# Optimization experiments

Hardware: AMD Instinct MI355X
Metric: run time of the kernel (lower is better)

The kernel has to match this reference:

```python
import jax, jax.numpy as jnp
import numpy as np

NEG_SLOPE = 0.01  # nn.LeakyReLU default


def _quantize_weight(w, bits):
    """Brevitas-style per-tensor symmetric narrow-range weight quantization.
    scale = max|w| / (2^(bits-1)-1); w_q = clip(round(w/scale)) * scale."""
    n = float(2 ** (bits - 1) - 1)
    scale = jnp.max(jnp.abs(w)) / n
    q = jnp.clip(jnp.round(w / scale), -n, n)
    return q * scale


def setup_inputs() -> dict:
    key = jax.random.key(0)
    ks = jax.random.split(key, 7)
    N, D_in, D_out = 32768, 1024, 2048
    x = jax.random.normal(ks[0], (N, D_in), dtype=jnp.float32)
    # He-ish init scaling for stability
    W0 = jax.random.normal(ks[1], (D_out, D_in), dtype=jnp.float32) * (1.0 / np.sqrt(D_in))
    b0 = jax.random.normal(ks[2], (D_out,), dtype=jnp.float32) * 0.01
    W1 = jax.random.normal(ks[3], (D_out, D_out), dtype=jnp.float32) * (1.0 / np.sqrt(D_out))
    b1 = jax.random.normal(ks[4], (D_out,), dtype=jnp.float32) * 0.01
    W2 = jax.random.normal(ks[5], (D_out, D_out), dtype=jnp.float32) * (1.0 / np.sqrt(D_out))
    b2 = jax.random.normal(ks[6], (D_out,), dtype=jnp.float32) * 0.01
    return {"x": x, "W0": W0, "b0": b0, "W1": W1, "b1": b1, "W2": W2, "b2": b2}


def reference(x, W0, b0, W1, b1, W2, b2):
    # Layer 0: QuantLinear with default 8-bit weights, then LeakyReLU, dropout(p=0)=id
    h = jnp.dot(x, _quantize_weight(W0, 8).T) + b0
    h = jnp.where(h >= 0, h, NEG_SLOPE * h)
    # Layers 1..2: 4-bit quantized weights
    for W, b in ((W1, b1), (W2, b2)):
        h = jnp.dot(h, _quantize_weight(W, 4).T) + b
        h = jnp.where(h >= 0, h, NEG_SLOPE * h)
    return h
```

## Files before the change

### kernel.cpp

```cpp
#include <hip/hip_runtime.h>
#include <hip/hip_bf16.h>
#include <stdint.h>

typedef __bf16 bf16x8 __attribute__((ext_vector_type(8)));
typedef float  f32x4  __attribute__((ext_vector_type(4)));
typedef unsigned short u16;

__device__ __forceinline__ u16 f2bf(float f) {
    return __builtin_bit_cast(u16, __float2bfloat16(f));
}

__device__ __forceinline__ void gload16(const void* g, void* l) {
    __builtin_amdgcn_global_load_lds(
        (const __attribute__((address_space(1))) void*)g,
        (__attribute__((address_space(3))) void*)l,
        16, 0, 0);
}


__global__ void zero3_k(unsigned int* p) {
    if (threadIdx.x < 3) p[threadIdx.x] = 0u;
}

__global__ void maxabs_k(const float* __restrict__ w, int n, unsigned int* __restrict__ out) {
    const int tid = threadIdx.x;
    float m = 0.f;
    for (int i = blockIdx.x * blockDim.x + tid; i < n; i += gridDim.x * blockDim.x)
        m = fmaxf(m, fabsf(w[i]));
    #pragma unroll
    for (int off = 32; off > 0; off >>= 1)
        m = fmaxf(m, __shfl_down(m, off));
    __shared__ float red[4];
    if ((tid & 63) == 0) red[tid >> 6] = m;
    __syncthreads();
    if (tid == 0) {
        m = fmaxf(fmaxf(red[0], red[1]), fmaxf(red[2], red[3]));
        atomicMax(out, __float_as_uint(m));
    }
}

__global__ void quant_k(const float* __restrict__ w, int n,
                        const unsigned int* __restrict__ maxbits, float qn,
                        u16* __restrict__ out) {
    const float scale = __uint_as_float(*maxbits) / qn;
    for (int i = blockIdx.x * blockDim.x + threadIdx.x; i < n; i += gridDim.x * blockDim.x) {
        float q = rintf(w[i] / scale);
        q = fminf(qn, fmaxf(-qn, q));
        out[i] = f2bf(q * scale);
    }
}

__global__ void cvt_k(const float* __restrict__ x, u16* __restrict__ o, long n) {
    const long stride = (long)gridDim.x * blockDim.x * 4;
    for (long i = ((long)blockIdx.x * blockDim.x + threadIdx.x) * 4; i < n; i += stride) {
        float4 v = *(const float4*)(x + i);
        unsigned int lo = (unsigned int)f2bf(v.x) | ((unsigned int)f2bf(v.y) << 16);
        unsigned int hi = (unsigned int)f2bf(v.z) | ((unsigned int)f2bf(v.w) << 16);
        *(uint2*)(o + i) = make_uint2(lo, hi);
    }
}


#define VM4   asm volatile("s_waitcnt vmcnt(4)" ::: "memory")
#define BARR  __builtin_amdgcn_s_barrier()
#define LGKM0 do { asm volatile("s_waitcnt lgkmcnt(0)" ::: "memory");          \
                   __builtin_amdgcn_sched_barrier(0); } while (0)
#define FENCE asm volatile("" ::: "memory")

#define STG(kt, ISA, h)                                                        \
  do {                                                                         \
    const u16* _s = (ISA) ? gA : gB;                                           \
    u16* _d = smem + ((ISA) ? 0 : 32768) + (((kt) & 1) << 14) + ((h) << 13)    \
              + wave * 512;                                                    \
    const size_t _go = (size_t)((h) * 128) * K + (size_t)(kt) * 64;            \
    gload16(_s + _go,                 _d);                                     \
    gload16(_s + _go + (size_t)64 * K, _d + 4096);                             \
  } while (0)

#define RD_A(kt, mh)                                                           \
  do {                                                                         \
    const u16* _p = smem + (((kt) & 1) << 14) + ((mh) << 13) + rowA;           \
    _Pragma("unroll") for (int m2 = 0; m2 < 4; ++m2) {                         \
        afr[m2 * 2]     = *(const bf16x8*)(_p + m2 * 2048 + g0);               \
        afr[m2 * 2 + 1] = *(const bf16x8*)(_p + m2 * 2048 + g1);               \
    }                                                                          \
  } while (0)

#define RD_B(kt, nh, DST)                                                      \
  do {                                                                         \
    const u16* _p = smem + 32768 + (((kt) & 1) << 14) + ((nh) << 13) + rowB;   \
    _Pragma("unroll") for (int n2 = 0; n2 < 2; ++n2) {                         \
        DST[n2 * 2]     = *(const bf16x8*)(_p + n2 * 4096 + g0);               \
        DST[n2 * 2 + 1] = *(const bf16x8*)(_p + n2 * 4096 + g1);               \
    }                                                                          \
  } while (0)

#define MM(mh, nh, BS)                                                         \
  do {                                                                         \
    __builtin_amdgcn_s_setprio(1);                                             \
    _Pragma("unroll") for (int m2 = 0; m2 < 4; ++m2)                           \
      _Pragma("unroll") for (int n2 = 0; n2 < 2; ++n2) {                       \
        acc[(mh)*4+m2][(nh)*2+n2] = __builtin_amdgcn_mfma_f32_16x16x32_bf16(   \
            afr[m2*2],     BS[n2*2],   acc[(mh)*4+m2][(nh)*2+n2], 0, 0, 0);    \
        acc[(mh)*4+m2][(nh)*2+n2] = __builtin_amdgcn_mfma_f32_16x16x32_bf16(   \
            afr[m2*2+1],   BS[n2*2+1], acc[(mh)*4+m2][(nh)*2+n2], 0, 0, 0);    \
      }                                                                        \
    __builtin_amdgcn_s_setprio(0);                                             \
  } while (0)

template<int BF16OUT>
__global__ __launch_bounds__(512, 2)
void gemm8x(const u16* __restrict__ A, const u16* __restrict__ B,
            const float* __restrict__ bias, void* __restrict__ Cv,
            int M, int Nn, int K)
{
    __shared__ __align__(128) u16 smem[65536];

    const int tid  = threadIdx.x;
    const int lane = tid & 63;
    const int wave = tid >> 6;
    const int wm = wave >> 2;
    const int wn = wave & 3;

    const int nbx = Nn >> 8;
    const int cpx = gridDim.x >> 3;
    const int swz = (blockIdx.x & 7) * cpx + (blockIdx.x >> 3);
    const int bn = (swz % nbx) << 8;
    const int bm = (swz / nbx) << 8;

    const int scol = (((tid & 7) ^ ((tid >> 4) & 7)) << 3);
    const u16* gA = A + (size_t)(bm + (tid >> 3)) * K + scol;
    const u16* gB = B + (size_t)(bn + (tid >> 3)) * K + scol;

    const int fr = lane & 15;
    const int g0 = (((lane >> 4)    ) ^ (fr >> 1)) << 3;
    const int g1 = (((lane >> 4) + 4) ^ (fr >> 1)) << 3;
    const int rowA = (wm * 16 + fr) << 6;
    const int rowB = (wn * 16 + fr) << 6;

    f32x4 acc[8][4] = {};
    bf16x8 afr[8], b0f[4], b1f[4];

    const int NT = K >> 6;

    STG(0, 1, 0); STG(0, 0, 0); STG(0, 0, 1); STG(0, 1, 1);
    VM4;
    BARR;

    for (int kt = 0; kt < NT - 1; ++kt) {
        RD_A(kt, 0); RD_B(kt, 0, b0f);
        STG(kt + 1, 1, 0);
        VM4; BARR; LGKM0;
        MM(0, 0, b0f);
        FENCE; BARR;
        RD_B(kt, 1, b1f);
        STG(kt + 1, 0, 0);
        VM4; BARR; LGKM0;
        MM(0, 1, b1f);
        FENCE; BARR;
        RD_A(kt, 1);
        STG(kt + 1, 0, 1);
        BARR; LGKM0;
        MM(1, 0, b0f);
        FENCE; BARR;
        STG(kt + 1, 1, 1);
        VM4; BARR;
        __builtin_amdgcn_sched_barrier(0);
        MM(1, 1, b1f);
        FENCE; BARR;
    }
    {
        const int kt = NT - 1;
        RD_A(kt, 0); RD_B(kt, 0, b0f);
        asm volatile("s_waitcnt vmcnt(2)" ::: "memory");
        BARR; LGKM0;
        MM(0, 0, b0f);
        FENCE; BARR;
        RD_B(kt, 1, b1f);
        asm volatile("s_waitcnt vmcnt(0)" ::: "memory");
        BARR; LGKM0;
        MM(0, 1, b1f);
        FENCE; BARR;
        RD_A(kt, 1);
        BARR; LGKM0;
        MM(1, 0, b0f);
        FENCE;
        __builtin_amdgcn_sched_barrier(0);
        MM(1, 1, b1f);
    }

    const int crow = (lane >> 4) << 2;
    const int ccol = lane & 15;
    #pragma unroll
    for (int n = 0; n < 4; ++n) {
        const int col = bn + n * 64 + wn * 16 + ccol;
        const float bv = bias[col];
        #pragma unroll
        for (int m = 0; m < 8; ++m) {
            const int row0 = bm + (m >> 2) * 128 + (m & 3) * 32 + wm * 16 + crow;
            #pragma unroll
            for (int j = 0; j < 4; ++j) {
                float v = acc[m][n][j] + bv;
                v = (v >= 0.f) ? v : 0.01f * v;
                if (BF16OUT) {
                    ((u16*)Cv)[(size_t)(row0 + j) * Nn + col] = f2bf(v);
                } else {
                    ((float*)Cv)[(size_t)(row0 + j) * Nn + col] = v;
                }
            }
        }
    }
}


extern "C" void kernel_launch(void* const* d_in, const int* in_sizes, int n_in,
                              void* d_out, int out_size, void* d_ws, size_t ws_size,
                              hipStream_t stream) {
    const float* x  = (const float*)d_in[0];
    const float* W0 = (const float*)d_in[1];
    const float* b0 = (const float*)d_in[2];
    const float* W1 = (const float*)d_in[3];
    const float* b1 = (const float*)d_in[4];
    const float* W2 = (const float*)d_in[5];
    const float* b2 = (const float*)d_in[6];

    const int N = 32768, D0 = 1024, D1 = 2048;

    char* ws = (char*)d_ws;
    u16* xbf = (u16*)ws;  ws += (size_t)N * D0 * 2;
    u16* h0  = (u16*)ws;  ws += (size_t)N * D1 * 2;
    u16* h1  = (u16*)ws;  ws += (size_t)N * D1 * 2;
    u16* w0q = (u16*)ws;  ws += (size_t)D1 * D0 * 2;
    u16* w1q = (u16*)ws;  ws += (size_t)D1 * D1 * 2;
    u16* w2q = (u16*)ws;  ws += (size_t)D1 * D1 * 2;
    unsigned int* scales = (unsigned int*)ws;

    zero3_k<<<1, 64, 0, stream>>>(scales);
    maxabs_k<<<256, 256, 0, stream>>>(W0, D1 * D0, scales + 0);
    maxabs_k<<<256, 256, 0, stream>>>(W1, D1 * D1, scales + 1);
    maxabs_k<<<256, 256, 0, stream>>>(W2, D1 * D1, scales + 2);
    quant_k<<<2048, 256, 0, stream>>>(W0, D1 * D0, scales + 0, 127.f, w0q);
    quant_k<<<2048, 256, 0, stream>>>(W1, D1 * D1, scales + 1, 7.f, w1q);
    quant_k<<<2048, 256, 0, stream>>>(W2, D1 * D1, scales + 2, 7.f, w2q);
    cvt_k<<<4096, 256, 0, stream>>>(x, xbf, (long)N * D0);

    const int blocks = (D1 / 256) * (N / 256);
    gemm8x<1><<<blocks, 512, 0, stream>>>(xbf, w0q, b0, h0, N, D1, D0);
    gemm8x<1><<<blocks, 512, 0, stream>>>(h0, w1q, b1, h1, N, D1, D1);
    gemm8x<0><<<blocks, 512, 0, stream>>>(h1, w2q, b2, d_out, N, D1, D1);
}
```

Baseline: 744.5 us.

## Restructure GEMM k-loop to prefetch whole next tile with two barriers per step

Replaces the fine-grained per-quarter staging schedule, which had about eight barriers per k-tile, with a simpler scheme. At the top of each k-tile the whole next tile is issued into the other LDS buffer, the kernel waits for the current tile's loads, and then all four MFMA quarters run back to back with only LDS waits between them. This cuts barrier and synchronisation overhead. In exchange, global loads now overlap with a full tile of compute rather than being interleaved, and all waves must reach the barrier before any staging starts.

Result: slower. 810.0 us (+8.8%).

```diff
diff --git a/kernel.cpp b/kernel.cpp
--- a/kernel.cpp
+++ b/kernel.cpp
@@ -61,7 +61,6 @@
 }
 
 
-#define VM4   asm volatile("s_waitcnt vmcnt(4)" ::: "memory")
 #define BARR  __builtin_amdgcn_s_barrier()
 #define LGKM0 do { asm volatile("s_waitcnt lgkmcnt(0)" ::: "memory");          \
                    __builtin_amdgcn_sched_barrier(0); } while (0)
@@ -108,6 +107,26 @@
     __builtin_amdgcn_s_setprio(0);                                             \
   } while (0)
 
+#define KTILE(kt, VMSTR, DO_STAGE)                                             \
+  do {                                                                         \
+    FENCE; BARR; FENCE;          \
+    if (DO_STAGE) { STG((kt)+1, 1, 0); STG((kt)+1, 0, 0);                      \
+                    STG((kt)+1, 0, 1); STG((kt)+1, 1, 1); }                    \
+    asm volatile("s_waitcnt vmcnt(" VMSTR ")" ::: "memory");                   \
+    FENCE; BARR; FENCE;          \
+    RD_A(kt, 0); RD_B(kt, 0, b0f);                                             \
+    LGKM0;                                                                     \
+    MM(0, 0, b0f);                                                             \
+    RD_B(kt, 1, b1f);                                                          \
+    LGKM0;                                                                     \
+    MM(0, 1, b1f);                                                             \
+    RD_A(kt, 1);                                                               \
+    LGKM0;                                                                     \
+    MM(1, 0, b0f);                                                             \
+    __builtin_amdgcn_sched_barrier(0);                                         \
+    MM(1, 1, b1f);                                                             \
+  } while (0)
+
 template<int BF16OUT>
 __global__ __launch_bounds__(512, 2)
 void gemm8x(const u16* __restrict__ A, const u16* __restrict__ B,
@@ -144,50 +163,10 @@
     const int NT = K >> 6;
 
     STG(0, 1, 0); STG(0, 0, 0); STG(0, 0, 1); STG(0, 1, 1);
-    VM4;
-    BARR;
-
-    for (int kt = 0; kt < NT - 1; ++kt) {
-        RD_A(kt, 0); RD_B(kt, 0, b0f);
-        STG(kt + 1, 1, 0);
-        VM4; BARR; LGKM0;
-        MM(0, 0, b0f);
-        FENCE; BARR;
-        RD_B(kt, 1, b1f);
-        STG(kt + 1, 0, 0);
-        VM4; BARR; LGKM0;
-        MM(0, 1, b1f);
-        FENCE; BARR;
-        RD_A(kt, 1);
-        STG(kt + 1, 0, 1);
-        BARR; LGKM0;
-        MM(1, 0, b0f);
-        FENCE; BARR;
-        STG(kt + 1, 1, 1);
-        VM4; BARR;
-        __builtin_amdgcn_sched_barrier(0);
-        MM(1, 1, b1f);
-        FENCE; BARR;
-    }
-    {
-        const int kt = NT - 1;
-        RD_A(kt, 0); RD_B(kt, 0, b0f);
-        asm volatile("s_waitcnt vmcnt(2)" ::: "memory");
-        BARR; LGKM0;
-        MM(0, 0, b0f);
-        FENCE; BARR;
-        RD_B(kt, 1, b1f);
-        asm volatile("s_waitcnt vmcnt(0)" ::: "memory");
-        BARR; LGKM0;
-        MM(0, 1, b1f);
-        FENCE; BARR;
-        RD_A(kt, 1);
-        BARR; LGKM0;
-        MM(1, 0, b0f);
-        FENCE;
-        __builtin_amdgcn_sched_barrier(0);
-        MM(1, 1, b1f);
-    }
+
+    for (int kt = 0; kt < NT - 1; ++kt)
+        KTILE(kt, "8", true);
+    KTILE(NT - 1, "0", false);
 
     const int crow = (lane >> 4) << 2;
     const int ccol = lane & 15;
```
